# Performance work log

Hardware: AMD Instinct MI355X
Metric: run time of the kernel (lower is better)

The kernel has to match this reference:

```python
import jax, jax.numpy as jnp
import numpy as np

N_NODES = 50000
N_EDGES = 800000
IN = 64
HID = 64
OUT = 12
N_LAYERS = 4
N_GRAPHS = 512


def setup_inputs() -> dict:
    key = jax.random.key(0)
    ks = jax.random.split(key, 20)
    s = 1.0 / np.sqrt(HID)
    inp = {
        "x": jax.random.normal(ks[0], (N_NODES, IN), dtype=jnp.float32),
        "edge_index": jax.random.randint(ks[1], (2, N_EDGES), 0, N_NODES, dtype=jnp.int32),
        "batch": jnp.sort(jax.random.randint(ks[2], (N_NODES,), 0, N_GRAPHS, dtype=jnp.int32)),
        "batch_size": N_GRAPHS,
        # stacked per-layer ResGatedGraphConv params (in == hidden so one stack works)
        "Wk": jax.random.normal(ks[3], (N_LAYERS, HID, HID), dtype=jnp.float32) * s,
        "bk": jnp.zeros((N_LAYERS, HID), dtype=jnp.float32),
        "Wq": jax.random.normal(ks[4], (N_LAYERS, HID, HID), dtype=jnp.float32) * s,
        "bq": jnp.zeros((N_LAYERS, HID), dtype=jnp.float32),
        "Wv": jax.random.normal(ks[5], (N_LAYERS, HID, HID), dtype=jnp.float32) * s,
        "bv": jnp.zeros((N_LAYERS, HID), dtype=jnp.float32),
        "Ws": jax.random.normal(ks[6], (N_LAYERS, HID, HID), dtype=jnp.float32) * s,
        "bs": jnp.zeros((N_LAYERS, HID), dtype=jnp.float32),
        "mlp_w1": jax.random.normal(ks[7], (HID, HID), dtype=jnp.float32) * s,
        "mlp_b1": jnp.zeros((HID,), dtype=jnp.float32),
        "mlp_w2": jax.random.normal(ks[8], (HID, OUT), dtype=jnp.float32) * s,
        "mlp_b2": jnp.zeros((OUT,), dtype=jnp.float32),
    }
    return inp


def _res_gated_conv(x, src, dst, wk, bk_, wq, bq_, wv, bv_, ws, bs_, n_nodes):
    # PyG ResGatedGraphConv: eta = sigmoid(key(x_i) + query(x_j)); agg_i = sum eta * value(x_j)
    k = x @ wk + bk_  # [N, H]
    q = x @ wq + bq_
    v = x @ wv + bv_
    gate = jax.nn.sigmoid(k[dst] + q[src])          # [E, H] gather + elementwise
    msg = gate * v[src]                              # [E, H]
    agg = jax.ops.segment_sum(msg, dst, num_segments=n_nodes)  # scatter-add
    return agg + x @ ws + bs_                        # root/skip connection


def reference(x, edge_index, batch, batch_size, Wk, bk, Wq, bq, Wv, bv, Ws, bs,
              mlp_w1, mlp_b1, mlp_w2, mlp_b2):
    src, dst = edge_index[0], edge_index[1]  # messages flow src(j) -> dst(i)
    n_nodes = x.shape[0]
    for l in range(N_LAYERS):
        x = _res_gated_conv(x, src, dst, Wk[l], bk[l], Wq[l], bq[l],
                            Wv[l], bv[l], Ws[l], bs[l], n_nodes)
        x = jax.nn.gelu(x, approximate=False)  # torch nn.GELU default = exact
    # global mean pool over graphs
    sums = jax.ops.segment_sum(x, batch, num_segments=batch_size)          # [B, H]
    cnts = jax.ops.segment_sum(jnp.ones((n_nodes,), x.dtype), batch,
                               num_segments=batch_size)                    # [B]
    pooled = sums / jnp.maximum(cnts, 1.0)[:, None]
    # MLP head: Linear -> ReLU -> (dropout off at inference) -> Linear
    h = jax.nn.relu(pooled @ mlp_w1 + mlp_b1)
    return h @ mlp_w2 + mlp_b2
```

## Files before the change

### kernel.cpp

```cpp
#include <hip/hip_runtime.h>
#include <math.h>

#define N_NODES  50000
#define N_EDGES  800000
#define HID      64
#define OUT_DIM  12
#define N_LAYERS 4
#define N_GRAPHS 512

#define SCAN_CHUNK 512
#define N_CHUNKS   ((N_NODES + SCAN_CHUNK - 1) / SCAN_CHUNK)

typedef unsigned short u16;
typedef unsigned int   u32;

__device__ __forceinline__ u16 f2bf(float f) {
    u32 u = __float_as_uint(f);
    u32 r = (u + 0x7FFFu + ((u >> 16) & 1u)) >> 16;
    return (u16)r;
}
__device__ __forceinline__ float bf2f(u32 h) {
    return __uint_as_float(h << 16);
}

__global__ __launch_bounds__(256) void gemm2m_kernel(
    const float* __restrict__ x,
    const float* __restrict__ Wq, const float* __restrict__ bq,
    const float* __restrict__ Wv, const float* __restrict__ bv,
    const float* __restrict__ Wk, const float* __restrict__ bk,
    const float* __restrict__ Ws, const float* __restrict__ bs,
    u32* __restrict__ qv, float* __restrict__ ok, float* __restrict__ os)
{
    __shared__ float xs[64][65];
    __shared__ float wsm[2][64][64];
    const int t = threadIdx.x;
    const int gbase = blockIdx.x * 64;

    const float *Wa, *ba, *Wb, *bb;
    if (blockIdx.y == 0) { Wa = Wq; ba = bq; Wb = Wv; bb = bv; }
    else                 { Wa = Wk; ba = bk; Wb = Ws; bb = bs; }

    #pragma unroll
    for (int i = 0; i < 4; ++i) {
        int idx = t + i * 256;
        int r   = idx >> 4;
        int c4  = idx & 15;
        int gn  = gbase + r;
        float4 val = make_float4(0.f, 0.f, 0.f, 0.f);
        if (gn < N_NODES) val = *(const float4*)(x + (size_t)gn * HID + c4 * 4);
        xs[r][c4 * 4 + 0] = val.x; xs[r][c4 * 4 + 1] = val.y;
        xs[r][c4 * 4 + 2] = val.z; xs[r][c4 * 4 + 3] = val.w;
        *(float4*)&wsm[0][r][c4 * 4] = *(const float4*)(Wa + r * HID + c4 * 4);
        *(float4*)&wsm[1][r][c4 * 4] = *(const float4*)(Wb + r * HID + c4 * 4);
    }
    __syncthreads();

    const int cg = (t & 15) * 4;
    const int ng = (t >> 4) * 4;

    float acc[2][4][4];
    {
        float4 ba4 = *(const float4*)(ba + cg);
        float4 bb4 = *(const float4*)(bb + cg);
        #pragma unroll
        for (int i = 0; i < 4; ++i) {
            acc[0][i][0] = ba4.x; acc[0][i][1] = ba4.y; acc[0][i][2] = ba4.z; acc[0][i][3] = ba4.w;
            acc[1][i][0] = bb4.x; acc[1][i][1] = bb4.y; acc[1][i][2] = bb4.z; acc[1][i][3] = bb4.w;
        }
    }

    #pragma unroll 8
    for (int k = 0; k < 64; ++k) {
        float xr[4];
        #pragma unroll
        for (int i = 0; i < 4; ++i) xr[i] = xs[ng + i][k];
        float4 wa = *(float4*)&wsm[0][k][cg];
        float4 wb = *(float4*)&wsm[1][k][cg];
        #pragma unroll
        for (int i = 0; i < 4; ++i) {
            acc[0][i][0] = fmaf(xr[i], wa.x, acc[0][i][0]);
            acc[0][i][1] = fmaf(xr[i], wa.y, acc[0][i][1]);
            acc[0][i][2] = fmaf(xr[i], wa.z, acc[0][i][2]);
            acc[0][i][3] = fmaf(xr[i], wa.w, acc[0][i][3]);
            acc[1][i][0] = fmaf(xr[i], wb.x, acc[1][i][0]);
            acc[1][i][1] = fmaf(xr[i], wb.y, acc[1][i][1]);
            acc[1][i][2] = fmaf(xr[i], wb.z, acc[1][i][2]);
            acc[1][i][3] = fmaf(xr[i], wb.w, acc[1][i][3]);
        }
    }

    if (blockIdx.y == 0) {
        #pragma unroll
        for (int i = 0; i < 4; ++i) {
            int gn = gbase + ng + i;
            if (gn < N_NODES) {
                u32 q01 = (u32)f2bf(acc[0][i][0]) | ((u32)f2bf(acc[0][i][1]) << 16);
                u32 q23 = (u32)f2bf(acc[0][i][2]) | ((u32)f2bf(acc[0][i][3]) << 16);
                u32 v01 = (u32)f2bf(acc[1][i][0]) | ((u32)f2bf(acc[1][i][1]) << 16);
                u32 v23 = (u32)f2bf(acc[1][i][2]) | ((u32)f2bf(acc[1][i][3]) << 16);
                *(uint4*)(qv + (size_t)gn * 64 + cg) = make_uint4(q01, v01, q23, v23);
            }
        }
    } else {
        #pragma unroll
        for (int i = 0; i < 4; ++i) {
            int gn = gbase + ng + i;
            if (gn < N_NODES) {
                size_t off = (size_t)gn * HID + cg;
                *(float4*)(ok + off) = make_float4(acc[0][i][0], acc[0][i][1], acc[0][i][2], acc[0][i][3]);
                *(float4*)(os + off) = make_float4(acc[1][i][0], acc[1][i][1], acc[1][i][2], acc[1][i][3]);
            }
        }
    }
}

__global__ __launch_bounds__(256) void hist_kernel(
    const int* __restrict__ ei, int* __restrict__ deg)
{
    int e = blockIdx.x * 256 + threadIdx.x;
    if (e < N_EDGES) atomicAdd(&deg[ei[N_EDGES + e]], 1);
}

__global__ __launch_bounds__(SCAN_CHUNK) void scan1_kernel(
    const int* __restrict__ deg, int* __restrict__ base, int* __restrict__ blocksum)
{
    __shared__ int s[SCAN_CHUNK];
    int t = threadIdx.x;
    int i = blockIdx.x * SCAN_CHUNK + t;
    int v = (i < N_NODES) ? deg[i] : 0;
    s[t] = v;
    __syncthreads();
    for (int off = 1; off < SCAN_CHUNK; off <<= 1) {
        int u = (t >= off) ? s[t - off] : 0;
        __syncthreads();
        s[t] += u;
        __syncthreads();
    }
    if (i < N_NODES) base[i] = s[t] - v;
    if (t == SCAN_CHUNK - 1) blocksum[blockIdx.x] = s[t];
}

__global__ __launch_bounds__(128) void scan2_kernel(
    const int* __restrict__ blocksum, int* __restrict__ blockoff)
{
    __shared__ int s[128];
    int t = threadIdx.x;
    int v = (t < N_CHUNKS) ? blocksum[t] : 0;
    s[t] = v;
    __syncthreads();
    for (int off = 1; off < 128; off <<= 1) {
        int u = (t >= off) ? s[t - off] : 0;
        __syncthreads();
        s[t] += u;
        __syncthreads();
    }
    if (t < N_CHUNKS) blockoff[t] = s[t] - v;
}

__global__ __launch_bounds__(SCAN_CHUNK) void scan3_kernel(
    int* __restrict__ base, const int* __restrict__ blockoff)
{
    int i = blockIdx.x * SCAN_CHUNK + threadIdx.x;
    if (i < N_NODES) base[i] += blockoff[blockIdx.x];
    if (i == 0) base[N_NODES] = N_EDGES;
}

__global__ __launch_bounds__(256) void scatter_kernel(
    const int* __restrict__ ei, const int* __restrict__ base,
    int* __restrict__ cursor, int* __restrict__ csr_src)
{
    int e = blockIdx.x * 256 + threadIdx.x;
    if (e >= N_EDGES) return;
    int s = ei[e];
    int d = ei[N_EDGES + e];
    int pos = base[d] + atomicAdd(&cursor[d], 1);
    csr_src[pos] = s;
}

__global__ __launch_bounds__(256) void agg_gelu_kernel(
    const int* __restrict__ base, const int* __restrict__ csr_src,
    const float* __restrict__ kf, const u32* __restrict__ qv,
    const float* __restrict__ skip, float* __restrict__ outx)
{
    int node = blockIdx.x * 4 + (threadIdx.x >> 6);
    if (node >= N_NODES) return;
    int lane = threadIdx.x & 63;
    int half = lane >> 5;
    int c    = lane & 31;

    float2 kd = *(const float2*)(kf + (size_t)node * HID + 2 * c);
    float acc0 = 0.f, acc1 = 0.f;
    int p0 = base[node];
    int p1 = base[node + 1];

    #pragma unroll 2
    for (int p = p0 + half; p < p1; p += 2) {
        int s = csr_src[p];
        uint2 qp = *(const uint2*)(qv + (size_t)s * 64 + 2 * c);
        float q0 = bf2f(qp.x & 0xffffu), q1 = bf2f(qp.x >> 16);
        float v0 = bf2f(qp.y & 0xffffu), v1 = bf2f(qp.y >> 16);
        float g0 = 1.f / (1.f + __expf(-(kd.x + q0)));
        float g1 = 1.f / (1.f + __expf(-(kd.y + q1)));
        acc0 = fmaf(g0, v0, acc0);
        acc1 = fmaf(g1, v1, acc1);
    }

    acc0 += __shfl_xor(acc0, 32);
    acc1 += __shfl_xor(acc1, 32);

    if (half == 0) {
        float2 sk = *(const float2*)(skip + (size_t)node * HID + 2 * c);
        float xo0 = acc0 + sk.x;
        float xo1 = acc1 + sk.y;
        float g0 = 0.5f * xo0 * (1.f + erff(xo0 * 0.70710678118f));
        float g1 = 0.5f * xo1 * (1.f + erff(xo1 * 0.70710678118f));
        *(float2*)(outx + (size_t)node * HID + 2 * c) = make_float2(g0, g1);
    }
}

__global__ __launch_bounds__(256) void bounds_kernel(
    const int* __restrict__ batch, int* __restrict__ start)
{
    int n = blockIdx.x * 256 + threadIdx.x;
    if (n >= N_NODES) return;
    int b  = batch[n];
    int bp = (n == 0) ? -1 : batch[n - 1];
    for (int g = bp + 1; g <= b; ++g) start[g] = n;
    if (n == N_NODES - 1) {
        for (int g = b + 1; g <= N_GRAPHS; ++g) start[g] = N_NODES;
    }
}

__global__ __launch_bounds__(256) void pool2_kernel(
    const float* __restrict__ x, const int* __restrict__ start,
    float* __restrict__ pooled)
{
    int g    = blockIdx.x;
    int lane = threadIdx.x & 63;
    int wid  = threadIdx.x >> 6;
    int s0 = start[g];
    int s1 = start[g + 1];
    float acc = 0.f;
    for (int n = s0 + wid; n < s1; n += 4)
        acc += x[(size_t)n * HID + lane];
    __shared__ float red[4][64];
    red[wid][lane] = acc;
    __syncthreads();
    if (wid == 0) {
        float s = red[0][lane] + red[1][lane] + red[2][lane] + red[3][lane];
        float cnt = fmaxf((float)(s1 - s0), 1.f);
        pooled[(size_t)g * HID + lane] = s / cnt;
    }
}

__global__ __launch_bounds__(64) void head_kernel(
    const float* __restrict__ pooled,
    const float* __restrict__ w1, const float* __restrict__ b1,
    const float* __restrict__ w2, const float* __restrict__ b2,
    float* __restrict__ out)
{
    int g = blockIdx.x;
    int t = threadIdx.x;
    __shared__ float p[64];
    __shared__ float h[64];
    p[t] = pooled[(size_t)g * HID + t];
    __syncthreads();
    float acc = b1[t];
    #pragma unroll 8
    for (int k = 0; k < HID; ++k) acc = fmaf(p[k], w1[k * HID + t], acc);
    h[t] = fmaxf(acc, 0.f);
    __syncthreads();
    if (t < OUT_DIM) {
        float a2 = b2[t];
        #pragma unroll 8
        for (int k = 0; k < HID; ++k) a2 = fmaf(h[k], w2[k * OUT_DIM + t], a2);
        out[(size_t)g * OUT_DIM + t] = a2;
    }
}

extern "C" void kernel_launch(void* const* d_in, const int* in_sizes, int n_in,
                              void* d_out, int out_size, void* d_ws, size_t ws_size,
                              hipStream_t stream)
{
    const float* x     = (const float*)d_in[0];
    const int*   ei    = (const int*)d_in[1];
    const int*   batch = (const int*)d_in[2];
    const float* Wk = (const float*)d_in[4];
    const float* bk = (const float*)d_in[5];
    const float* Wq = (const float*)d_in[6];
    const float* bq = (const float*)d_in[7];
    const float* Wv = (const float*)d_in[8];
    const float* bv = (const float*)d_in[9];
    const float* Ws = (const float*)d_in[10];
    const float* bs = (const float*)d_in[11];
    const float* w1 = (const float*)d_in[12];
    const float* b1 = (const float*)d_in[13];
    const float* w2 = (const float*)d_in[14];
    const float* b2 = (const float*)d_in[15];
    float* out = (float*)d_out;

    char* wsb = (char*)d_ws;
    const size_t NF = (size_t)N_NODES * HID;
    float* bufA   = (float*)wsb;                    wsb += NF * 4;
    float* bufB   = (float*)wsb;                    wsb += NF * 4;
    float* bufK   = (float*)wsb;                    wsb += NF * 4;
    u32*   bufQV  = (u32*)wsb;                      wsb += NF * 4;
    float* pooled = (float*)wsb;                    wsb += (size_t)N_GRAPHS * HID * 4;
    int*   baseI  = (int*)wsb;                      wsb += (N_NODES + 1) * 4;
    int*   csr_src= (int*)wsb;                      wsb += (size_t)N_EDGES * 4;
    int*   startI = (int*)wsb;                      wsb += (N_GRAPHS + 1) * 4;
    int* deg      = (int*)bufB;
    int* cursor   = deg + N_NODES;
    int* blocksum = cursor + N_NODES;
    int* blockoff = blocksum + 128;

    const int gemm_gx = (N_NODES + 63) / 64;
    const int eg      = (N_EDGES + 255) / 256;
    const int agg_g   = (N_NODES + 3) / 4;
    const int nd_g    = (N_NODES + 255) / 256;

    hipMemsetAsync(deg, 0, (size_t)2 * N_NODES * sizeof(int), stream);
    hist_kernel<<<eg, 256, 0, stream>>>(ei, deg);
    scan1_kernel<<<N_CHUNKS, SCAN_CHUNK, 0, stream>>>(deg, baseI, blocksum);
    scan2_kernel<<<1, 128, 0, stream>>>(blocksum, blockoff);
    scan3_kernel<<<N_CHUNKS, SCAN_CHUNK, 0, stream>>>(baseI, blockoff);
    scatter_kernel<<<eg, 256, 0, stream>>>(ei, baseI, cursor, csr_src);
    bounds_kernel<<<nd_g, 256, 0, stream>>>(batch, startI);

    const float* xsrc = x;
    for (int l = 0; l < N_LAYERS; ++l) {
        float* sb = (l & 1) ? bufB : bufA;
        gemm2m_kernel<<<dim3(gemm_gx, 2), 256, 0, stream>>>(
            xsrc,
            Wq + (size_t)l * HID * HID, bq + (size_t)l * HID,
            Wv + (size_t)l * HID * HID, bv + (size_t)l * HID,
            Wk + (size_t)l * HID * HID, bk + (size_t)l * HID,
            Ws + (size_t)l * HID * HID, bs + (size_t)l * HID,
            bufQV, bufK, sb);
        agg_gelu_kernel<<<agg_g, 256, 0, stream>>>(
            baseI, csr_src, bufK, bufQV, sb, sb);
        xsrc = sb;
    }

    pool2_kernel<<<N_GRAPHS, 256, 0, stream>>>(xsrc, startI, pooled);
    head_kernel<<<N_GRAPHS, 64, 0, stream>>>(pooled, w1, b1, w2, b2, out);
}
```

Measured before the change: 413.6 us.

## Use bf16 MFMA for node projections and store activations in bf16

Replaces the fp32 FMA projection GEMM with bf16 MFMA 16x16x32 instructions. Weights are pre-transposed and converted to bf16 by a prep kernel, and the input is converted once. Layer outputs are now written as bf16, which halves activation traffic for the GEMM, aggregation writes and pooling. CSR construction records each edge's atomic rank during the histogram, so the scatter pass needs no second atomic. This adds bf16 rounding to activations and weights, and the MFMA kernel does uncoalesced scalar stores for the k/skip outputs.

```diff
diff --git a/kernel.cpp b/kernel.cpp
--- a/kernel.cpp
+++ b/kernel.cpp
@@ -13,112 +13,146 @@
 
 typedef unsigned short u16;
 typedef unsigned int   u32;
-
-__device__ __forceinline__ u16 f2bf(float f) {
+typedef __attribute__((ext_vector_type(8))) short bf16x8;
+typedef __attribute__((ext_vector_type(4))) float f32x4;
+
+__device__ __forceinline__ u32 f2bf(float f) {
     u32 u = __float_as_uint(f);
-    u32 r = (u + 0x7FFFu + ((u >> 16) & 1u)) >> 16;
-    return (u16)r;
+    return (u + 0x7FFFu + ((u >> 16) & 1u)) >> 16;
 }
 __device__ __forceinline__ float bf2f(u32 h) {
     return __uint_as_float(h << 16);
 }
 
-__global__ __launch_bounds__(256) void gemm2m_kernel(
-    const float* __restrict__ x,
-    const float* __restrict__ Wq, const float* __restrict__ bq,
-    const float* __restrict__ Wv, const float* __restrict__ bv,
-    const float* __restrict__ Wk, const float* __restrict__ bk,
-    const float* __restrict__ Ws, const float* __restrict__ bs,
+__global__ __launch_bounds__(256) void wprep_kernel(
+    const float* __restrict__ Wq, const float* __restrict__ Wv,
+    const float* __restrict__ Wk, const float* __restrict__ Ws,
+    u16* __restrict__ wt)
+{
+    int m = blockIdx.x;
+    int lyr = m >> 2, j = m & 3;
+    const float* src;
+    switch (j) { case 0: src = Wq; break; case 1: src = Wv; break;
+                 case 2: src = Wk; break; default: src = Ws; }
+    src += (size_t)lyr * HID * HID;
+    int t  = threadIdx.x;
+    int n  = t >> 2;
+    int k0 = (t & 3) * 16;
+    u32 buf[8];
+    #pragma unroll
+    for (int i = 0; i < 16; i += 2) {
+        float f0 = src[(k0 + i) * HID + n];
+        float f1 = src[(k0 + i + 1) * HID + n];
+        buf[i / 2] = f2bf(f0) | (f2bf(f1) << 16);
+    }
+    u32* dst = (u32*)(wt + (size_t)m * 4096 + n * 64 + k0);
+    *(uint4*)(dst)     = make_uint4(buf[0], buf[1], buf[2], buf[3]);
+    *(uint4*)(dst + 4) = make_uint4(buf[4], buf[5], buf[6], buf[7]);
+}
+
+__global__ __launch_bounds__(256) void cvt_kernel(
+    const float* __restrict__ x, u32* __restrict__ xbf)
+{
+    int i = blockIdx.x * 256 + threadIdx.x;
+    if (i >= N_NODES * HID / 8) return;
+    float4 a = ((const float4*)x)[2 * i];
+    float4 b = ((const float4*)x)[2 * i + 1];
+    ((uint4*)xbf)[i] = make_uint4(
+        f2bf(a.x) | (f2bf(a.y) << 16), f2bf(a.z) | (f2bf(a.w) << 16),
+        f2bf(b.x) | (f2bf(b.y) << 16), f2bf(b.z) | (f2bf(b.w) << 16));
+}
+
+__global__ __launch_bounds__(256) void gemm_mfma_kernel(
+    const u16* __restrict__ xbf, const u16* __restrict__ wt, int layer,
+    const float* __restrict__ bq, const float* __restrict__ bv,
+    const float* __restrict__ bk, const float* __restrict__ bs,
     u32* __restrict__ qv, float* __restrict__ ok, float* __restrict__ os)
 {
-    __shared__ float xs[64][65];
-    __shared__ float wsm[2][64][64];
     const int t = threadIdx.x;
+    const int w = t >> 6;
+    const int l = t & 63;
+    const int row16 = l & 15;
+    const int kgrp  = l >> 4;
     const int gbase = blockIdx.x * 64;
 
-    const float *Wa, *ba, *Wb, *bb;
-    if (blockIdx.y == 0) { Wa = Wq; ba = bq; Wb = Wv; bb = bv; }
-    else                 { Wa = Wk; ba = bk; Wb = Ws; bb = bs; }
-
-    #pragma unroll
-    for (int i = 0; i < 4; ++i) {
-        int idx = t + i * 256;
-        int r   = idx >> 4;
-        int c4  = idx & 15;
-        int gn  = gbase + r;
-        float4 val = make_float4(0.f, 0.f, 0.f, 0.f);
-        if (gn < N_NODES) val = *(const float4*)(x + (size_t)gn * HID + c4 * 4);
-        xs[r][c4 * 4 + 0] = val.x; xs[r][c4 * 4 + 1] = val.y;
-        xs[r][c4 * 4 + 2] = val.z; xs[r][c4 * 4 + 3] = val.w;
-        *(float4*)&wsm[0][r][c4 * 4] = *(const float4*)(Wa + r * HID + c4 * 4);
-        *(float4*)&wsm[1][r][c4 * 4] = *(const float4*)(Wb + r * HID + c4 * 4);
-    }
-    __syncthreads();
-
-    const int cg = (t & 15) * 4;
-    const int ng = (t >> 4) * 4;
-
-    float acc[2][4][4];
-    {
-        float4 ba4 = *(const float4*)(ba + cg);
-        float4 bb4 = *(const float4*)(bb + cg);
-        #pragma unroll
-        for (int i = 0; i < 4; ++i) {
-            acc[0][i][0] = ba4.x; acc[0][i][1] = ba4.y; acc[0][i][2] = ba4.z; acc[0][i][3] = ba4.w;
-            acc[1][i][0] = bb4.x; acc[1][i][1] = bb4.y; acc[1][i][2] = bb4.z; acc[1][i][3] = bb4.w;
-        }
-    }
-
-    #pragma unroll 8
-    for (int k = 0; k < 64; ++k) {
-        float xr[4];
-        #pragma unroll
-        for (int i = 0; i < 4; ++i) xr[i] = xs[ng + i][k];
-        float4 wa = *(float4*)&wsm[0][k][cg];
-        float4 wb = *(float4*)&wsm[1][k][cg];
-        #pragma unroll
-        for (int i = 0; i < 4; ++i) {
-            acc[0][i][0] = fmaf(xr[i], wa.x, acc[0][i][0]);
-            acc[0][i][1] = fmaf(xr[i], wa.y, acc[0][i][1]);
-            acc[0][i][2] = fmaf(xr[i], wa.z, acc[0][i][2]);
-            acc[0][i][3] = fmaf(xr[i], wa.w, acc[0][i][3]);
-            acc[1][i][0] = fmaf(xr[i], wb.x, acc[1][i][0]);
-            acc[1][i][1] = fmaf(xr[i], wb.y, acc[1][i][1]);
-            acc[1][i][2] = fmaf(xr[i], wb.z, acc[1][i][2]);
-            acc[1][i][3] = fmaf(xr[i], wb.w, acc[1][i][3]);
-        }
+    const u16 *wA, *wB; const float *bA, *bB;
+    if (blockIdx.y == 0) { wA = wt + (size_t)(layer * 4 + 0) * 4096; bA = bq;
+                           wB = wt + (size_t)(layer * 4 + 1) * 4096; bB = bv; }
+    else                 { wA = wt + (size_t)(layer * 4 + 2) * 4096; bA = bk;
+                           wB = wt + (size_t)(layer * 4 + 3) * 4096; bB = bs; }
+
+    int nodeA = gbase + w * 16 + row16;
+    int nodeAc = nodeA < N_NODES ? nodeA : N_NODES - 1;
+    bf16x8 a0 = *(const bf16x8*)(xbf + (size_t)nodeAc * 64 + kgrp * 8);
+    bf16x8 a1 = *(const bf16x8*)(xbf + (size_t)nodeAc * 64 + 32 + kgrp * 8);
+
+    f32x4 acc[2][4];
+    #pragma unroll
+    for (int nt = 0; nt < 4; ++nt) {
+        float fa = bA[nt * 16 + row16];
+        float fb = bB[nt * 16 + row16];
+        acc[0][nt] = (f32x4){fa, fa, fa, fa};
+        acc[1][nt] = (f32x4){fb, fb, fb, fb};
+    }
+
+    #pragma unroll
+    for (int nt = 0; nt < 4; ++nt) {
+        const u16* pa = wA + (nt * 16 + row16) * 64 + kgrp * 8;
+        const u16* pb = wB + (nt * 16 + row16) * 64 + kgrp * 8;
+        bf16x8 ba0 = *(const bf16x8*)(pa);
+        bf16x8 ba1 = *(const bf16x8*)(pa + 32);
+        bf16x8 bb0 = *(const bf16x8*)(pb);
+        bf16x8 bb1 = *(const bf16x8*)(pb + 32);
+        acc[0][nt] = __builtin_amdgcn_mfma_f32_16x16x32_bf16(a0, ba0, acc[0][nt], 0, 0, 0);
+        acc[0][nt] = __builtin_amdgcn_mfma_f32_16x16x32_bf16(a1, ba1, acc[0][nt], 0, 0, 0);
+        acc[1][nt] = __builtin_amdgcn_mfma_f32_16x16x32_bf16(a0, bb0, acc[1][nt], 0, 0, 0);
+        acc[1][nt] = __builtin_amdgcn_mfma_f32_16x16x32_bf16(a1, bb1, acc[1][nt], 0, 0, 0);
     }
 
     if (blockIdx.y == 0) {
         #pragma unroll
-        for (int i = 0; i < 4; ++i) {
-            int gn = gbase + ng + i;
-            if (gn < N_NODES) {
-                u32 q01 = (u32)f2bf(acc[0][i][0]) | ((u32)f2bf(acc[0][i][1]) << 16);
-                u32 q23 = (u32)f2bf(acc[0][i][2]) | ((u32)f2bf(acc[0][i][3]) << 16);
-                u32 v01 = (u32)f2bf(acc[1][i][0]) | ((u32)f2bf(acc[1][i][1]) << 16);
-                u32 v23 = (u32)f2bf(acc[1][i][2]) | ((u32)f2bf(acc[1][i][3]) << 16);
-                *(uint4*)(qv + (size_t)gn * 64 + cg) = make_uint4(q01, v01, q23, v23);
+        for (int nt = 0; nt < 4; ++nt) {
+            #pragma unroll
+            for (int r = 0; r < 4; ++r) {
+                float qe = acc[0][nt][r];
+                float qo = __shfl_xor(qe, 1);
+                float ve = acc[1][nt][r];
+                float vo = __shfl_xor(ve, 1);
+                if (!(l & 1)) {
+                    int gn = gbase + w * 16 + kgrp * 4 + r;
+                    if (gn < N_NODES) {
+                        u32 qp = f2bf(qe) | (f2bf(qo) << 16);
+                        u32 vp = f2bf(ve) | (f2bf(vo) << 16);
+                        *(uint2*)(qv + (size_t)gn * 64 + nt * 16 + row16) = make_uint2(qp, vp);
+                    }
+                }
             }
         }
     } else {
         #pragma unroll
-        for (int i = 0; i < 4; ++i) {
-            int gn = gbase + ng + i;
-            if (gn < N_NODES) {
-                size_t off = (size_t)gn * HID + cg;
-                *(float4*)(ok + off) = make_float4(acc[0][i][0], acc[0][i][1], acc[0][i][2], acc[0][i][3]);
-                *(float4*)(os + off) = make_float4(acc[1][i][0], acc[1][i][1], acc[1][i][2], acc[1][i][3]);
+        for (int nt = 0; nt < 4; ++nt) {
+            #pragma unroll
+            for (int r = 0; r < 4; ++r) {
+                int gn = gbase + w * 16 + kgrp * 4 + r;
+                if (gn < N_NODES) {
+                    int col = nt * 16 + row16;
+                    ok[(size_t)gn * 64 + col] = acc[0][nt][r];
+                    os[(size_t)gn * 64 + col] = acc[1][nt][r];
+                }
             }
         }
     }
 }
 
 __global__ __launch_bounds__(256) void hist_kernel(
-    const int* __restrict__ ei, int* __restrict__ deg)
-{
-    int e = blockIdx.x * 256 + threadIdx.x;
-    if (e < N_EDGES) atomicAdd(&deg[ei[N_EDGES + e]], 1);
+    const int* __restrict__ ei, int* __restrict__ deg, int* __restrict__ rank)
+{
+    int e0 = (blockIdx.x * 256 + threadIdx.x) * 4;
+    #pragma unroll
+    for (int i = 0; i < 4; ++i) {
+        int e = e0 + i;
+        if (e < N_EDGES) rank[e] = atomicAdd(&deg[ei[N_EDGES + e]], 1);
+    }
 }
 
 __global__ __launch_bounds__(SCAN_CHUNK) void scan1_kernel(
@@ -167,20 +201,21 @@
 
 __global__ __launch_bounds__(256) void scatter_kernel(
     const int* __restrict__ ei, const int* __restrict__ base,
-    int* __restrict__ cursor, int* __restrict__ csr_src)
-{
-    int e = blockIdx.x * 256 + threadIdx.x;
-    if (e >= N_EDGES) return;
-    int s = ei[e];
-    int d = ei[N_EDGES + e];
-    int pos = base[d] + atomicAdd(&cursor[d], 1);
-    csr_src[pos] = s;
+    const int* __restrict__ rank, int* __restrict__ csr_src)
+{
+    int e0 = (blockIdx.x * 256 + threadIdx.x) * 4;
+    #pragma unroll
+    for (int i = 0; i < 4; ++i) {
+        int e = e0 + i;
+        if (e < N_EDGES)
+            csr_src[base[ei[N_EDGES + e]] + rank[e]] = ei[e];
+    }
 }
 
 __global__ __launch_bounds__(256) void agg_gelu_kernel(
     const int* __restrict__ base, const int* __restrict__ csr_src,
     const float* __restrict__ kf, const u32* __restrict__ qv,
-    const float* __restrict__ skip, float* __restrict__ outx)
+    const float* __restrict__ skip, u32* __restrict__ outxbf)
 {
     int node = blockIdx.x * 4 + (threadIdx.x >> 6);
     if (node >= N_NODES) return;
@@ -214,7 +249,7 @@
         float xo1 = acc1 + sk.y;
         float g0 = 0.5f * xo0 * (1.f + erff(xo0 * 0.70710678118f));
         float g1 = 0.5f * xo1 * (1.f + erff(xo1 * 0.70710678118f));
-        *(float2*)(outx + (size_t)node * HID + 2 * c) = make_float2(g0, g1);
+        outxbf[(size_t)node * 32 + c] = f2bf(g0) | (f2bf(g1) << 16);
     }
 }
 
@@ -232,24 +267,30 @@
 }
 
 __global__ __launch_bounds__(256) void pool2_kernel(
-    const float* __restrict__ x, const int* __restrict__ start,
+    const u32* __restrict__ xbf, const int* __restrict__ start,
     float* __restrict__ pooled)
 {
-    int g    = blockIdx.x;
-    int lane = threadIdx.x & 63;
-    int wid  = threadIdx.x >> 6;
+    int g   = blockIdx.x;
+    int t   = threadIdx.x;
+    int nid = t >> 5;
+    int c   = t & 31;
     int s0 = start[g];
     int s1 = start[g + 1];
-    float acc = 0.f;
-    for (int n = s0 + wid; n < s1; n += 4)
-        acc += x[(size_t)n * HID + lane];
-    __shared__ float red[4][64];
-    red[wid][lane] = acc;
-    __syncthreads();
-    if (wid == 0) {
-        float s = red[0][lane] + red[1][lane] + red[2][lane] + red[3][lane];
+    float a0 = 0.f, a1 = 0.f;
+    for (int n = s0 + nid; n < s1; n += 8) {
+        u32 p = xbf[(size_t)n * 32 + c];
+        a0 += bf2f(p & 0xffffu);
+        a1 += bf2f(p >> 16);
+    }
+    __shared__ float red0[8][32], red1[8][32];
+    red0[nid][c] = a0; red1[nid][c] = a1;
+    __syncthreads();
+    if (nid == 0) {
+        float t0 = 0.f, t1 = 0.f;
+        #pragma unroll
+        for (int i = 0; i < 8; ++i) { t0 += red0[i][c]; t1 += red1[i][c]; }
         float cnt = fmaxf((float)(s1 - s0), 1.f);
-        pooled[(size_t)g * HID + lane] = s / cnt;
+        *(float2*)(pooled + (size_t)g * HID + 2 * c) = make_float2(t0 / cnt, t1 / cnt);
     }
 }
 
@@ -301,47 +342,46 @@
 
     char* wsb = (char*)d_ws;
     const size_t NF = (size_t)N_NODES * HID;
-    float* bufA   = (float*)wsb;                    wsb += NF * 4;
-    float* bufB   = (float*)wsb;                    wsb += NF * 4;
+    u32*   xbf    = (u32*)wsb;                      wsb += NF * 2;
     float* bufK   = (float*)wsb;                    wsb += NF * 4;
+    float* bufS   = (float*)wsb;                    wsb += NF * 4;
     u32*   bufQV  = (u32*)wsb;                      wsb += NF * 4;
+    u16*   wt     = (u16*)wsb;                      wsb += (size_t)16 * 4096 * 2;
     float* pooled = (float*)wsb;                    wsb += (size_t)N_GRAPHS * HID * 4;
     int*   baseI  = (int*)wsb;                      wsb += (N_NODES + 1) * 4;
     int*   csr_src= (int*)wsb;                      wsb += (size_t)N_EDGES * 4;
     int*   startI = (int*)wsb;                      wsb += (N_GRAPHS + 1) * 4;
-    int* deg      = (int*)bufB;
-    int* cursor   = deg + N_NODES;
-    int* blocksum = cursor + N_NODES;
+    int* deg      = (int*)bufS;
+    int* rank     = deg + N_NODES;
+    int* blocksum = rank + N_EDGES;
     int* blockoff = blocksum + 128;
 
     const int gemm_gx = (N_NODES + 63) / 64;
-    const int eg      = (N_EDGES + 255) / 256;
-    const int agg_g   = (N_NODES + 3) / 4;
+    const int e4g     = (N_EDGES / 4 + 255) / 256;
+    const int agg_gx  = (N_NODES + 3) / 4;
     const int nd_g    = (N_NODES + 255) / 256;
-
-    hipMemsetAsync(deg, 0, (size_t)2 * N_NODES * sizeof(int), stream);
-    hist_kernel<<<eg, 256, 0, stream>>>(ei, deg);
+    const int cvt_g   = ((int)(NF / 8) + 255) / 256;
+
+    hipMemsetAsync(deg, 0, (size_t)N_NODES * sizeof(int), stream);
+    wprep_kernel<<<16, 256, 0, stream>>>(Wq, Wv, Wk, Ws, wt);
+    cvt_kernel<<<cvt_g, 256, 0, stream>>>(x, xbf);
+    hist_kernel<<<e4g, 256, 0, stream>>>(ei, deg, rank);
     scan1_kernel<<<N_CHUNKS, SCAN_CHUNK, 0, stream>>>(deg, baseI, blocksum);
     scan2_kernel<<<1, 128, 0, stream>>>(blocksum, blockoff);
     scan3_kernel<<<N_CHUNKS, SCAN_CHUNK, 0, stream>>>(baseI, blockoff);
-    scatter_kernel<<<eg, 256, 0, stream>>>(ei, baseI, cursor, csr_src);
+    scatter_kernel<<<e4g, 256, 0, stream>>>(ei, baseI, rank, csr_src);
     bounds_kernel<<<nd_g, 256, 0, stream>>>(batch, startI);
 
-    const float* xsrc = x;
     for (int l = 0; l < N_LAYERS; ++l) {
-        float* sb = (l & 1) ? bufB : bufA;
-        gemm2m_kernel<<<dim3(gemm_gx, 2), 256, 0, stream>>>(
-            xsrc,
-            Wq + (size_t)l * HID * HID, bq + (size_t)l * HID,
-            Wv + (size_t)l * HID * HID, bv + (size_t)l * HID,
-            Wk + (size_t)l * HID * HID, bk + (size_t)l * HID,
-            Ws + (size_t)l * HID * HID, bs + (size_t)l * HID,
-            bufQV, bufK, sb);
-        agg_gelu_kernel<<<agg_g, 256, 0, stream>>>(
-            baseI, csr_src, bufK, bufQV, sb, sb);
-        xsrc = sb;
-    }
-
-    pool2_kernel<<<N_GRAPHS, 256, 0, stream>>>(xsrc, startI, pooled);
+        gemm_mfma_kernel<<<dim3(gemm_gx, 2), 256, 0, stream>>>(
+            (const u16*)xbf, wt, l,
+            bq + (size_t)l * HID, bv + (size_t)l * HID,
+            bk + (size_t)l * HID, bs + (size_t)l * HID,
+            bufQV, bufK, bufS);
+        agg_gelu_kernel<<<agg_gx, 256, 0, stream>>>(
+            baseI, csr_src, bufK, bufQV, bufS, xbf);
+    }
+
+    pool2_kernel<<<N_GRAPHS, 256, 0, stream>>>(xbf, startI, pooled);
     head_kernel<<<N_GRAPHS, 64, 0, stream>>>(pooled, w1, b1, w2, b2, out);
 }
```

Measured after the change: 354.0 us. -14.4%, faster.
